# Kernel optimization log

Measured on AMD Instinct MI355X. Metric: run time of the kernel, lower is better.

Reference implementation:

```python
import jax, jax.numpy as jnp
import numpy as np
from jax import lax

LR, SB, LB = 256, 16, 8  # lr_size, spatial_bin, luma_bins
DN = ('NCHW', 'OIHW', 'NCHW')


def conv2d(x, w, b=None, stride=1, pad=1):
    out = lax.conv_general_dilated(x, w, (stride, stride), [(pad, pad), (pad, pad)], dimension_numbers=DN)
    return out if b is None else out + b[None, :, None, None]


def gaussian_blur17(x):
    # kornia GaussianBlur2d(kernel=(17,17), sigma=(2,2)), reflect padding, separable
    t = jnp.arange(17, dtype=x.dtype) - 8.0
    g = jnp.exp(-(t * t) / 8.0)  # 2*sigma^2 = 8
    g = g / g.sum()
    C = x.shape[1]
    xp = jnp.pad(x, ((0, 0), (0, 0), (8, 8), (8, 8)), mode='reflect')
    kh = jnp.broadcast_to(g.reshape(1, 1, 17, 1), (C, 1, 17, 1))
    kw = jnp.broadcast_to(g.reshape(1, 1, 1, 17), (C, 1, 1, 17))
    x1 = lax.conv_general_dilated(xp, kh, (1, 1), 'VALID', dimension_numbers=DN, feature_group_count=C)
    return lax.conv_general_dilated(x1, kw, (1, 1), 'VALID', dimension_numbers=DN, feature_group_count=C)


def nearest_resize(x, size):
    # torch F.interpolate mode='nearest': src = floor(dst * in/out)
    H, W = x.shape[-2], x.shape[-1]
    iy = jnp.floor(jnp.arange(size) * (H / size)).astype(jnp.int32)
    ix = jnp.floor(jnp.arange(size) * (W / size)).astype(jnp.int32)
    return x[:, :, iy][:, :, :, ix]


def grid_sample_3d_border(inp, grid):
    # inp [B,C,D,Hi,Wi]; grid [B,Do,Ho,Wo,3] with (x,y,z); bilinear, padding_mode='border', align_corners=False
    B, C, D, Hi, Wi = inp.shape
    x = jnp.clip(((grid[..., 0] + 1.0) * Wi - 1.0) * 0.5, 0.0, Wi - 1.0)
    y = jnp.clip(((grid[..., 1] + 1.0) * Hi - 1.0) * 0.5, 0.0, Hi - 1.0)
    z = jnp.clip(((grid[..., 2] + 1.0) * D - 1.0) * 0.5, 0.0, D - 1.0)
    x0 = jnp.floor(x); y0 = jnp.floor(y); z0 = jnp.floor(z)
    fx = (x - x0)[:, None]; fy = (y - y0)[:, None]; fz = (z - z0)[:, None]  # [B,1,Do,Ho,Wo]
    x0i = x0.astype(jnp.int32); y0i = y0.astype(jnp.int32); z0i = z0.astype(jnp.int32)
    x1i = jnp.minimum(x0i + 1, Wi - 1); y1i = jnp.minimum(y0i + 1, Hi - 1); z1i = jnp.minimum(z0i + 1, D - 1)
    flat = inp.reshape(B, C, D * Hi * Wi)
    M = grid.shape[1] * grid.shape[2] * grid.shape[3]

    def gat(zi, yi, xi):
        idx = ((zi * Hi + yi) * Wi + xi).reshape(B, 1, M)
        v = jnp.take_along_axis(flat, jnp.broadcast_to(idx, (B, C, M)), axis=2)
        return v.reshape(B, C, grid.shape[1], grid.shape[2], grid.shape[3])

    return (gat(z0i, y0i, x0i) * (1 - fz) * (1 - fy) * (1 - fx)
            + gat(z0i, y0i, x1i) * (1 - fz) * (1 - fy) * fx
            + gat(z0i, y1i, x0i) * (1 - fz) * fy * (1 - fx)
            + gat(z0i, y1i, x1i) * (1 - fz) * fy * fx
            + gat(z1i, y0i, x0i) * fz * (1 - fy) * (1 - fx)
            + gat(z1i, y0i, x1i) * fz * (1 - fy) * fx
            + gat(z1i, y1i, x0i) * fz * fy * (1 - fx)
            + gat(z1i, y1i, x1i) * fz * fy * fx)


def _forward(lqs, evs, gw1, gb1, gw2, gb2, sw0, sb0, sw1, sb1, sw2, sb2, sw3, sb3,
             cw0, cb0, cw1, cb1, fw1, fb1, fw2, fb2, fw3, fb3, lw1, lb1, lw2, fuw, fub):
    B, _, H, W = lqs.shape
    # --- HighresStreamNet guide ---
    g = gaussian_blur17(lqs)
    g = jax.nn.relu(conv2d(g, gw1, gb1, 1, 0))
    guide = jax.nn.sigmoid(conv2d(g, gw2, gb2, 1, 0)) * 2.0 - 0.5  # [B,1,H,W]
    # --- slicing grid (x,y in (-0.5,1.5) per source, z = guide) ---
    gx = (jnp.arange(W, dtype=lqs.dtype) + 0.5) / W * 2.0 - 0.5
    gy = (jnp.arange(H, dtype=lqs.dtype) + 0.5) / H * 2.0 - 0.5
    gyy, gxx = jnp.meshgrid(gy, gx, indexing='ij')
    base = jnp.broadcast_to(jnp.stack([gxx, gyy], -1)[None, None], (B, 1, H, W, 2))
    grid = jnp.concatenate([base, guide[..., None]], axis=-1)  # [B,1,H,W,3]
    # --- LowresStreamNet ---
    lr = nearest_resize(lqs, LR)
    ev = evs if (evs.shape[-1] == LR and evs.shape[-2] == LR) else nearest_resize(evs, LR)
    x = jnp.concatenate([lr, ev], axis=1)  # [B,18,256,256]
    for w_, b_ in ((sw0, sb0), (sw1, sb1), (sw2, sb2), (sw3, sb3)):
        x = jax.nn.relu(conv2d(x, w_, b_, 2, 1))  # -> [B,64,16,16]
    xl = conv2d(jax.nn.relu(conv2d(x, lw1, lb1, 1, 1)), lw2, None, 1, 1)  # local, last conv no bias
    xg = jax.nn.relu(conv2d(x, cw0, cb0, 2, 1))
    xg = jax.nn.relu(conv2d(xg, cw1, cb1, 2, 1)).reshape(B, -1)  # [B,1024]
    xg = jax.nn.relu(xg @ fw1.T + fb1)
    xg = jax.nn.relu(xg @ fw2.T + fb2)
    xg = xg @ fw3.T + fb3  # [B,64]
    fused = jax.nn.relu(xg[:, :, None, None] + xl)
    bg = conv2d(fused, fuw, fub, 1, 0).reshape(B, 1, LB, SB, SB)  # bilateral grid [B,1,8,16,16]
    hr = grid_sample_3d_border(bg, grid)  # [B,1,1,H,W]
    return hr.reshape(B, -1, H, W)


def setup_inputs():
    key = jax.random.key(0)
    ks = iter(jax.random.split(key, 40))

    def W_(shape):
        fan_in = int(np.prod(shape[1:]))
        return jax.random.normal(next(ks), shape, jnp.float32) * np.float32(np.sqrt(2.0 / fan_in))

    def Z(n):
        return jnp.zeros((n,), jnp.float32)

    B, H, Wd = 8, 1024, 1024
    return {
        'lqs': jax.random.uniform(next(ks), (B, 3, H, Wd), jnp.float32),
        'evs': jax.random.normal(next(ks), (B, 15, 256, 256), jnp.float32) * 0.1,
        'gw1': W_((16, 3, 1, 1)), 'gb1': Z(16), 'gw2': W_((1, 16, 1, 1)), 'gb2': Z(1),
        'sw0': W_((8, 18, 3, 3)), 'sb0': Z(8), 'sw1': W_((16, 8, 3, 3)), 'sb1': Z(16),
        'sw2': W_((32, 16, 3, 3)), 'sb2': Z(32), 'sw3': W_((64, 32, 3, 3)), 'sb3': Z(64),
        'cw0': W_((64, 64, 3, 3)), 'cb0': Z(64), 'cw1': W_((64, 64, 3, 3)), 'cb1': Z(64),
        'fw1': W_((256, 1024)), 'fb1': Z(256), 'fw2': W_((128, 256)), 'fb2': Z(128),
        'fw3': W_((64, 128)), 'fb3': Z(64),
        'lw1': W_((64, 64, 3, 3)), 'lb1': Z(64), 'lw2': W_((64, 64, 3, 3)),
        'fuw': W_((8, 64, 1, 1)), 'fub': Z(8),
    }


def reference(lqs, evs, gw1, gb1, gw2, gb2, sw0, sb0, sw1, sb1, sw2, sb2, sw3, sb3,
              cw0, cb0, cw1, cb1, fw1, fb1, fw2, fb2, fw3, fb3, lw1, lb1, lw2, fuw, fub):
    return _forward(lqs, evs, gw1, gb1, gw2, gb2, sw0, sb0, sw1, sb1, sw2, sb2, sw3, sb3,
                    cw0, cb0, cw1, cb1, fw1, fb1, fw2, fb2, fw3, fb3, lw1, lb1, lw2, fuw, fub)
```

## Files before the change

### kernel.cpp

```cpp
#include <hip/hip_runtime.h>
#include <hip/hip_bf16.h>
#include <math.h>

#define BATCH 8
#define HH 1024
#define WW 1024

__device__ __forceinline__ int reflect1024(int i) {
    i = i < 0 ? -i : i;
    return i > 1023 ? 2046 - i : i;
}

__global__ __launch_bounds__(256) void conv0_k(const float* __restrict__ lqs,
                                               const float* __restrict__ evs,
                                               const float* __restrict__ w,
                                               const float* __restrict__ bias,
                                               float* __restrict__ out) {
    int idx = blockIdx.x * 256 + threadIdx.x;
    int q = idx & 4095;
    int b = idx >> 12;
    int qx = q & 31, oy = q >> 5;
    int iy0 = oy * 2 - 1;

    float acc[4][8];
#pragma unroll
    for (int j = 0; j < 4; ++j)
#pragma unroll
        for (int o = 0; o < 8; ++o) acc[j][o] = bias[o];

#pragma unroll
    for (int ic = 0; ic < 3; ++ic) {
        const float* ipc = lqs + (size_t)(b * 3 + ic) * HH * WW;
#pragma unroll
        for (int ky = 0; ky < 3; ++ky) {
            int iy = iy0 + ky;
            if (iy < 0) continue;
            const float* row = ipc + (size_t)iy * 4 * WW;
            float xr[9];
#pragma unroll
            for (int i = 0; i < 9; ++i) {
                int ix = 8 * qx - 1 + i;
                xr[i] = (ix >= 0) ? row[ix * 4] : 0.0f;
            }
#pragma unroll
            for (int o = 0; o < 8; ++o) {
                const float* wp = w + (o * 18 + ic) * 9 + ky * 3;
#pragma unroll
                for (int j = 0; j < 4; ++j)
#pragma unroll
                    for (int kx = 0; kx < 3; ++kx)
                        acc[j][o] = fmaf(wp[kx], xr[2 * j + kx], acc[j][o]);
            }
        }
    }
    for (int ic = 0; ic < 15; ++ic) {
        const float* ipc = evs + (size_t)(b * 15 + ic) * 65536;
#pragma unroll
        for (int ky = 0; ky < 3; ++ky) {
            int iy = iy0 + ky;
            if (iy < 0) continue;
            const float* row = ipc + iy * 256;
            const float4* r4 = (const float4*)row;
            float4 A = r4[2 * qx];
            float4 Bv = r4[2 * qx + 1];
            float m = (qx > 0) ? row[8 * qx - 1] : 0.0f;
            float xr[9] = {m, A.x, A.y, A.z, A.w, Bv.x, Bv.y, Bv.z, Bv.w};
#pragma unroll
            for (int o = 0; o < 8; ++o) {
                const float* wp = w + (o * 18 + ic + 3) * 9 + ky * 3;
#pragma unroll
                for (int j = 0; j < 4; ++j)
#pragma unroll
                    for (int kx = 0; kx < 3; ++kx)
                        acc[j][o] = fmaf(wp[kx], xr[2 * j + kx], acc[j][o]);
            }
        }
    }
#pragma unroll
    for (int o = 0; o < 8; ++o) {
        float4 v = make_float4(fmaxf(acc[0][o], 0.0f), fmaxf(acc[1][o], 0.0f),
                               fmaxf(acc[2][o], 0.0f), fmaxf(acc[3][o], 0.0f));
        *(float4*)(out + ((size_t)(b * 8 + o) << 14) + oy * 128 + qx * 4) = v;
    }
}

template <int IC, int OC, int OCT, int IH, int IW, int STRIDE, bool RELU, bool HASB>
__global__ __launch_bounds__(256) void convN_k(const float* __restrict__ in,
                                               const float* __restrict__ w,
                                               const float* __restrict__ bias,
                                               float* __restrict__ out) {
    constexpr int OH = (IH + 2 - 3) / STRIDE + 1;
    constexpr int OW = (IW + 2 - 3) / STRIDE + 1;
    constexpr int POS = OH * OW;
    constexpr int G = OC / OCT;
    int idx = blockIdx.x * 256 + threadIdx.x;
    if (idx >= BATCH * G * POS) return;
    int px = idx % POS;
    int g = (idx / POS) % G;
    int b = idx / (POS * G);
    int ox = px % OW, oy = px / OW;
    int iy0 = oy * STRIDE - 1, ix0 = ox * STRIDE - 1;

    float acc[OCT];
#pragma unroll
    for (int o = 0; o < OCT; ++o) acc[o] = HASB ? bias[g * OCT + o] : 0.0f;

    const float* ip = in + (size_t)b * IC * IH * IW;
    for (int ic = 0; ic < IC; ++ic) {
        const float* ipc = ip + ic * IH * IW;
        float x[9];
#pragma unroll
        for (int ky = 0; ky < 3; ++ky) {
            int iy = iy0 + ky;
#pragma unroll
            for (int kx = 0; kx < 3; ++kx) {
                int ix = ix0 + kx;
                bool ok = (iy >= 0) && (iy < IH) && (ix >= 0) && (ix < IW);
                x[ky * 3 + kx] = ok ? ipc[iy * IW + ix] : 0.0f;
            }
        }
#pragma unroll
        for (int o = 0; o < OCT; ++o) {
            const float* wp = w + ((g * OCT + o) * IC + ic) * 9;
#pragma unroll
            for (int k = 0; k < 9; ++k) acc[o] = fmaf(wp[k], x[k], acc[o]);
        }
    }
#pragma unroll
    for (int o = 0; o < OCT; ++o) {
        float v = acc[o];
        if (RELU) v = fmaxf(v, 0.0f);
        out[(size_t)(b * OC + g * OCT + o) * POS + px] = v;
    }
}

template <int IC, int OC, int OCT, int IH, int IW, int STRIDE, int SPLIT>
__global__ __launch_bounds__(256) void convS_k(const float* __restrict__ in,
                                               const float* __restrict__ w,
                                               float* __restrict__ part) {
    constexpr int OH = (IH + 2 - 3) / STRIDE + 1;
    constexpr int OW = (IW + 2 - 3) / STRIDE + 1;
    constexpr int POS = OH * OW;
    constexpr int G = OC / OCT;
    constexpr int TOT = BATCH * G * POS;
    constexpr int ICS = IC / SPLIT;
    constexpr int N = BATCH * OC * POS;
    int idx = blockIdx.x * 256 + threadIdx.x;
    if (idx >= TOT * SPLIT) return;
    int s = idx / TOT, r = idx % TOT;
    int px = r % POS;
    int g = (r / POS) % G;
    int b = r / (POS * G);
    int ox = px % OW, oy = px / OW;
    int iy0 = oy * STRIDE - 1, ix0 = ox * STRIDE - 1;

    float acc[OCT];
#pragma unroll
    for (int o = 0; o < OCT; ++o) acc[o] = 0.0f;

    const float* ip = in + (size_t)b * IC * IH * IW;
    for (int ic = s * ICS; ic < (s + 1) * ICS; ++ic) {
        const float* ipc = ip + ic * IH * IW;
        float x[9];
#pragma unroll
        for (int ky = 0; ky < 3; ++ky) {
            int iy = iy0 + ky;
#pragma unroll
            for (int kx = 0; kx < 3; ++kx) {
                int ix = ix0 + kx;
                bool ok = (iy >= 0) && (iy < IH) && (ix >= 0) && (ix < IW);
                x[ky * 3 + kx] = ok ? ipc[iy * IW + ix] : 0.0f;
            }
        }
#pragma unroll
        for (int o = 0; o < OCT; ++o) {
            const float* wp = w + ((g * OCT + o) * IC + ic) * 9;
#pragma unroll
            for (int k = 0; k < 9; ++k) acc[o] = fmaf(wp[k], x[k], acc[o]);
        }
    }
#pragma unroll
    for (int o = 0; o < OCT; ++o)
        part[(size_t)s * N + (size_t)(b * OC + g * OCT + o) * POS + px] = acc[o];
}

template <int OC, int POS, int SPLIT, bool RELU, bool HASB>
__global__ __launch_bounds__(256) void reduce_k(const float* __restrict__ part,
                                                const float* __restrict__ bias,
                                                float* __restrict__ out) {
    constexpr int N = BATCH * OC * POS;
    int idx = blockIdx.x * 256 + threadIdx.x;
    if (idx >= N) return;
    int oc = (idx / POS) % OC;
    float a = HASB ? bias[oc] : 0.0f;
#pragma unroll
    for (int s = 0; s < SPLIT; ++s) a += part[(size_t)s * N + idx];
    out[idx] = RELU ? fmaxf(a, 0.0f) : a;
}

__global__ __launch_bounds__(256) void fc1_k(const float* __restrict__ part_cw1,
                                             const float* __restrict__ cb1,
                                             const float* __restrict__ fw1,
                                             const float* __restrict__ fb1,
                                             float* __restrict__ h1) {
    __shared__ float xin[1024];
    int t = threadIdx.x;
    int b = blockIdx.x >> 6;
    int rgrp = blockIdx.x & 63;
    int wave = t >> 6, lane = t & 63;

    for (int i = t; i < 1024; i += 256) {
        float v = cb1[i >> 4];
#pragma unroll
        for (int s = 0; s < 16; ++s) v += part_cw1[s * 8192 + b * 1024 + i];
        xin[i] = fmaxf(v, 0.0f);
    }
    __syncthreads();

    int r = (rgrp << 2) | wave;
    const float4* w4 = (const float4*)(fw1 + r * 1024);
    const float4* x4 = (const float4*)xin;
    float acc = 0.0f;
#pragma unroll
    for (int jj = 0; jj < 4; ++jj) {
        float4 wv = w4[lane + 64 * jj];
        float4 xv = x4[lane + 64 * jj];
        acc = fmaf(wv.x, xv.x, acc);
        acc = fmaf(wv.y, xv.y, acc);
        acc = fmaf(wv.z, xv.z, acc);
        acc = fmaf(wv.w, xv.w, acc);
    }
#pragma unroll
    for (int m = 32; m; m >>= 1) acc += __shfl_xor(acc, m, 64);
    if (lane == 0) h1[b * 256 + r] = fmaxf(acc + fb1[r], 0.0f);
}

__global__ __launch_bounds__(256) void fc2_k(const float* __restrict__ h1,
                                             const float* __restrict__ fw2,
                                             const float* __restrict__ fb2,
                                             float* __restrict__ h2) {
    int t = threadIdx.x;
    int b = blockIdx.x >> 5;
    int rgrp = blockIdx.x & 31;
    int wave = t >> 6, lane = t & 63;
    int r = (rgrp << 2) | wave;
    float4 wv = ((const float4*)(fw2 + r * 256))[lane];
    float4 xv = ((const float4*)(h1 + b * 256))[lane];
    float acc = fmaf(wv.x, xv.x, fmaf(wv.y, xv.y, fmaf(wv.z, xv.z, wv.w * xv.w)));
#pragma unroll
    for (int m = 32; m; m >>= 1) acc += __shfl_xor(acc, m, 64);
    if (lane == 0) h2[b * 128 + r] = fmaxf(acc + fb2[r], 0.0f);
}

__global__ __launch_bounds__(256) void fc3_k(const float* __restrict__ h2,
                                             const float* __restrict__ fw3,
                                             const float* __restrict__ fb3,
                                             float* __restrict__ xgv) {
    int t = threadIdx.x;
    int b = blockIdx.x >> 4;
    int rgrp = blockIdx.x & 15;
    int wave = t >> 6, lane = t & 63;
    int r = (rgrp << 2) | wave;
    float2 wv = ((const float2*)(fw3 + r * 128))[lane];
    float2 xv = ((const float2*)(h2 + b * 128))[lane];
    float acc = fmaf(wv.x, xv.x, wv.y * xv.y);
#pragma unroll
    for (int m = 32; m; m >>= 1) acc += __shfl_xor(acc, m, 64);
    if (lane == 0) xgv[b * 64 + r] = acc + fb3[r];
}

__global__ __launch_bounds__(256) void fuse_k(const float* __restrict__ xg,
                                              const float* __restrict__ part_lw2,
                                              const float* __restrict__ fuw,
                                              const float* __restrict__ fub,
                                              float* __restrict__ bg) {
    int px = threadIdx.x;
    int d = blockIdx.x & 7;
    int b = blockIdx.x >> 3;
    float acc = fub[d];
    for (int c = 0; c < 64; ++c) {
        int base = (b * 64 + c) * 256 + px;
        float xlv = 0.0f;
#pragma unroll
        for (int s = 0; s < 8; ++s) xlv += part_lw2[s * 131072 + base];
        float f = fmaxf(xg[b * 64 + c] + xlv, 0.0f);
        acc = fmaf(fuw[d * 64 + c], f, acc);
    }
    bg[(b * 8 + d) * 256 + px] = acc;
}

__global__ __launch_bounds__(256) void guide_slice_k(const float* __restrict__ lqs,
                                                     const float* __restrict__ bgp,
                                                     const float* __restrict__ gw1,
                                                     const float* __restrict__ gb1,
                                                     const float* __restrict__ gw2,
                                                     const float* __restrict__ gb2,
                                                     float* __restrict__ out) {
    constexpr int TW = 64, TH = 32;
    __shared__ float sBH[3][TH][81];
    __shared__ float sBG[2048];
    __shared__ float sW1[48], sB1[16], sW2[16], sB2v[1];

    int t = threadIdx.x;
    int bx = blockIdx.x & 15;
    int by = (blockIdx.x >> 4) & 31;
    int b = blockIdx.x >> 9;
    int x0 = bx * TW, y0 = by * TH;

    float gv[17];
    {
        float gs = 0.0f;
#pragma unroll
        for (int i = 0; i < 17; ++i) {
            float d = (float)i - 8.0f;
            gv[i] = expf(-(d * d) * 0.125f);
            gs += gv[i];
        }
        float inv = 1.0f / gs;
#pragma unroll
        for (int i = 0; i < 17; ++i) gv[i] *= inv;
    }

    for (int i = t; i < 2048; i += 256) sBG[i] = bgp[b * 2048 + i];
    if (t < 48) sW1[t] = gw1[t];
    if (t < 16) { sB1[t] = gb1[t]; sW2[t] = gw2[t]; }
    if (t == 0) sB2v[0] = gb2[0];

    if (t < 240) {
        int c = t / 80, xo = t % 80;
        int gx = reflect1024(x0 + xo - 8);
        const float* colp = lqs + (size_t)(b * 3 + c) * HH * WW + gx;
        float win[17];
#pragma unroll
        for (int i = 0; i < 16; ++i)
            win[i] = colp[(size_t)reflect1024(y0 - 8 + i) * WW];
#pragma unroll
        for (int j = 0; j < TH; ++j) {
            win[(16 + j) % 17] = colp[(size_t)reflect1024(y0 + 8 + j) * WW];
            float acc = 0.0f;
#pragma unroll
            for (int i = 0; i < 17; ++i) acc = fmaf(gv[i], win[(j + i) % 17], acc);
            sBH[c][j][xo] = acc;
        }
    }
    __syncthreads();

    int yy = t >> 3, xs = (t & 7) * 8;
    int Y = y0 + yy;
    float fy = fminf(fmaxf((Y + 0.5f) * (1.0f / 64.0f) + 3.5f, 0.0f), 15.0f);
    float yf = floorf(fy);
    int yi = (int)yf;
    float ay = fy - yf;
    int yi1 = min(yi + 1, 15);

    float bcv[3][8];
#pragma unroll
    for (int c = 0; c < 3; ++c) {
        float win[17];
#pragma unroll
        for (int i = 0; i < 16; ++i) win[i] = sBH[c][yy][xs + i];
#pragma unroll
        for (int j = 0; j < 8; ++j) {
            win[(16 + j) % 17] = sBH[c][yy][xs + 16 + j];
            float acc = 0.0f;
#pragma unroll
            for (int i = 0; i < 17; ++i) acc = fmaf(gv[i], win[(j + i) % 17], acc);
            bcv[c][j] = acc;
        }
    }

    float val[8];
#pragma unroll
    for (int j = 0; j < 8; ++j) {
        float b0 = bcv[0][j], b1 = bcv[1][j], b2 = bcv[2][j];
        float s = sB2v[0];
#pragma unroll
        for (int c = 0; c < 16; ++c) {
            float g1 = fmaf(sW1[c * 3 + 0], b0,
                       fmaf(sW1[c * 3 + 1], b1,
                       fmaf(sW1[c * 3 + 2], b2, sB1[c])));
            s = fmaf(sW2[c], fmaxf(g1, 0.0f), s);
        }
        float sig = 1.0f / (1.0f + expf(-s));
        float guide = sig * 2.0f - 0.5f;

        int X = x0 + xs + j;
        float fx = fminf(fmaxf((X + 0.5f) * (1.0f / 64.0f) + 3.5f, 0.0f), 15.0f);
        float fz = fminf(fmaxf(fmaf(guide, 4.0f, 3.5f), 0.0f), 7.0f);
        float xf = floorf(fx), zf = floorf(fz);
        int xi = (int)xf, zi = (int)zf;
        float ax = fx - xf, az = fz - zf;
        int xi1 = min(xi + 1, 15), zi1 = min(zi + 1, 7);

        const float* g0 = sBG + zi * 256;
        const float* g1p = sBG + zi1 * 256;
        int i00 = yi * 16 + xi, i01 = yi * 16 + xi1;
        int i10 = yi1 * 16 + xi, i11 = yi1 * 16 + xi1;
        float c00 = g0[i00] + az * (g1p[i00] - g0[i00]);
        float c01 = g0[i01] + az * (g1p[i01] - g0[i01]);
        float c10 = g0[i10] + az * (g1p[i10] - g0[i10]);
        float c11 = g0[i11] + az * (g1p[i11] - g0[i11]);
        float c0 = c00 + ay * (c10 - c00);
        float c1 = c01 + ay * (c11 - c01);
        val[j] = c0 + ax * (c1 - c0);
    }
    float4* op = (float4*)(out + (size_t)b * HH * WW + (size_t)Y * WW + x0 + xs);
    op[0] = make_float4(val[0], val[1], val[2], val[3]);
    op[1] = make_float4(val[4], val[5], val[6], val[7]);
}

extern "C" void kernel_launch(void* const* d_in, const int* in_sizes, int n_in,
                              void* d_out, int out_size, void* d_ws, size_t ws_size,
                              hipStream_t stream) {
    const float* lqs = (const float*)d_in[0];
    const float* evs = (const float*)d_in[1];
    const float* gw1 = (const float*)d_in[2];
    const float* gb1 = (const float*)d_in[3];
    const float* gw2 = (const float*)d_in[4];
    const float* gb2 = (const float*)d_in[5];
    const float* sw0 = (const float*)d_in[6];
    const float* sb0 = (const float*)d_in[7];
    const float* sw1 = (const float*)d_in[8];
    const float* sb1 = (const float*)d_in[9];
    const float* sw2 = (const float*)d_in[10];
    const float* sb2 = (const float*)d_in[11];
    const float* sw3 = (const float*)d_in[12];
    const float* sb3 = (const float*)d_in[13];
    const float* cw0 = (const float*)d_in[14];
    const float* cb0 = (const float*)d_in[15];
    const float* cw1 = (const float*)d_in[16];
    const float* cb1 = (const float*)d_in[17];
    const float* fw1 = (const float*)d_in[18];
    const float* fb1 = (const float*)d_in[19];
    const float* fw2 = (const float*)d_in[20];
    const float* fb2 = (const float*)d_in[21];
    const float* fw3 = (const float*)d_in[22];
    const float* fb3 = (const float*)d_in[23];
    const float* lw1 = (const float*)d_in[24];
    const float* lb1 = (const float*)d_in[25];
    const float* lw2 = (const float*)d_in[26];
    const float* fuw = (const float*)d_in[27];
    const float* fub = (const float*)d_in[28];
    float* out = (float*)d_out;

    float* ws = (float*)d_ws;
    float* o0 = ws;
    float* o1 = o0 + 1048576;
    float* o2 = o1 + 524288;
    float* o3 = o2 + 262144;
    float* xl1 = o3 + 131072;
    float* xg0 = xl1 + 131072;
    float* xgv = xg0 + 32768;
    float* bg = xgv + 512;
    float* h1 = bg + 16384;
    float* h2 = h1 + 2048;
    float* partA = h2 + 1024;
    float* part_lw2 = partA + 1048576;
    float* part_cw1 = part_lw2 + 1048576;

    conv0_k<<<128, 256, 0, stream>>>(lqs, evs, sw0, sb0, o0);
    convN_k<8, 16, 8, 128, 128, 2, true, true><<<256, 256, 0, stream>>>(o0, sw1, sb1, o1);
    convS_k<16, 32, 8, 64, 64, 2, 4><<<512, 256, 0, stream>>>(o1, sw2, partA);
    reduce_k<32, 1024, 4, true, true><<<1024, 256, 0, stream>>>(partA, sb2, o2);
    convS_k<32, 64, 8, 32, 32, 2, 8><<<512, 256, 0, stream>>>(o2, sw3, partA);
    reduce_k<64, 256, 8, true, true><<<512, 256, 0, stream>>>(partA, sb3, o3);
    convS_k<64, 64, 8, 16, 16, 1, 8><<<512, 256, 0, stream>>>(o3, lw1, partA);
    reduce_k<64, 256, 8, true, true><<<512, 256, 0, stream>>>(partA, lb1, xl1);
    convS_k<64, 64, 8, 16, 16, 1, 8><<<512, 256, 0, stream>>>(xl1, lw2, part_lw2);
    convS_k<64, 64, 8, 16, 16, 2, 16><<<256, 256, 0, stream>>>(o3, cw0, partA);
    reduce_k<64, 64, 16, true, true><<<128, 256, 0, stream>>>(partA, cb0, xg0);
    convS_k<64, 64, 4, 8, 8, 2, 16><<<128, 256, 0, stream>>>(xg0, cw1, part_cw1);
    fc1_k<<<512, 256, 0, stream>>>(part_cw1, cb1, fw1, fb1, h1);
    fc2_k<<<256, 256, 0, stream>>>(h1, fw2, fb2, h2);
    fc3_k<<<128, 256, 0, stream>>>(h2, fw3, fb3, xgv);
    fuse_k<<<64, 256, 0, stream>>>(xgv, part_lw2, fuw, fub, bg);
    guide_slice_k<<<BATCH * 32 * 16, 256, 0, stream>>>(lqs, bg, gw1, gb1, gw2, gb2, out);
}
```

Before: 397.2 us.

## Fuse low-res conv/FC pipeline into one cooperative persistent kernel with grid syncs

Replaces the chain of sixteen small conv, split-reduce, FC and fuse kernels with a single cooperative kernel of 512 blocks that runs each stage and separates them with grid-wide syncs. The split-K partial buffers and reduce kernels are removed; each thread now computes full-IC outputs with fewer output channels per thread. The FC layers and fuse step run inside eight blocks using shared memory. This targets launch overhead and the extra partial-sum traffic, but gives up parallelism in later stages and adds grid-sync cost.

```diff
diff --git a/kernel.cpp b/kernel.cpp
--- a/kernel.cpp
+++ b/kernel.cpp
@@ -1,153 +1,93 @@
 #include <hip/hip_runtime.h>
+#include <hip/hip_cooperative_groups.h>
 #include <hip/hip_bf16.h>
 #include <math.h>
+
+namespace cg = cooperative_groups;
 
 #define BATCH 8
 #define HH 1024
 #define WW 1024
 
+#define NBLK 512
+#define NTHR 131072
+
 __device__ __forceinline__ int reflect1024(int i) {
     i = i < 0 ? -i : i;
     return i > 1023 ? 2046 - i : i;
 }
 
-__global__ __launch_bounds__(256) void conv0_k(const float* __restrict__ lqs,
-                                               const float* __restrict__ evs,
-                                               const float* __restrict__ w,
-                                               const float* __restrict__ bias,
-                                               float* __restrict__ out) {
-    int idx = blockIdx.x * 256 + threadIdx.x;
-    int q = idx & 4095;
-    int b = idx >> 12;
-    int qx = q & 31, oy = q >> 5;
-    int iy0 = oy * 2 - 1;
-
-    float acc[4][8];
-#pragma unroll
-    for (int j = 0; j < 4; ++j)
-#pragma unroll
-        for (int o = 0; o < 8; ++o) acc[j][o] = bias[o];
+struct MegaArgs {
+    const float *lqs, *evs;
+    const float *sw0, *sb0, *sw1, *sb1, *sw2, *sb2, *sw3, *sb3;
+    const float *lw1, *lb1, *lw2;
+    const float *cw0, *cb0, *cw1, *cb1;
+    const float *fw1, *fb1, *fw2, *fb2, *fw3, *fb3;
+    const float *fuw, *fub;
+    float *o0, *o1, *o2, *o3, *xl1, *xl2, *xg0, *xin, *bg;
+};
+
+__device__ __forceinline__ void stage_conv0(int idx, const MegaArgs& A) {
+    int px = idx & 16383;
+    int b = idx >> 14;
+    int ox = px & 127, oy = px >> 7;
+    int iy0 = 2 * oy - 1, ix0 = 2 * ox - 1;
+
+    float acc[8];
+#pragma unroll
+    for (int o = 0; o < 8; ++o) acc[o] = A.sb0[o];
 
 #pragma unroll
     for (int ic = 0; ic < 3; ++ic) {
-        const float* ipc = lqs + (size_t)(b * 3 + ic) * HH * WW;
+        const float* ipc = A.lqs + ((size_t)(b * 3 + ic) << 20);
 #pragma unroll
         for (int ky = 0; ky < 3; ++ky) {
             int iy = iy0 + ky;
-            if (iy < 0) continue;
+            if ((unsigned)iy >= 256u) continue;
             const float* row = ipc + (size_t)iy * 4 * WW;
-            float xr[9];
-#pragma unroll
-            for (int i = 0; i < 9; ++i) {
-                int ix = 8 * qx - 1 + i;
-                xr[i] = (ix >= 0) ? row[ix * 4] : 0.0f;
-            }
-#pragma unroll
-            for (int o = 0; o < 8; ++o) {
-                const float* wp = w + (o * 18 + ic) * 9 + ky * 3;
-#pragma unroll
-                for (int j = 0; j < 4; ++j)
-#pragma unroll
-                    for (int kx = 0; kx < 3; ++kx)
-                        acc[j][o] = fmaf(wp[kx], xr[2 * j + kx], acc[j][o]);
+#pragma unroll
+            for (int kx = 0; kx < 3; ++kx) {
+                int ix = ix0 + kx;
+                if ((unsigned)ix >= 256u) continue;
+                float v = row[ix * 4];
+                const float* wp = A.sw0 + ic * 9 + ky * 3 + kx;
+#pragma unroll
+                for (int o = 0; o < 8; ++o) acc[o] = fmaf(wp[o * 162], v, acc[o]);
             }
         }
     }
     for (int ic = 0; ic < 15; ++ic) {
-        const float* ipc = evs + (size_t)(b * 15 + ic) * 65536;
+        const float* ipc = A.evs + ((size_t)(b * 15 + ic) << 16);
 #pragma unroll
         for (int ky = 0; ky < 3; ++ky) {
             int iy = iy0 + ky;
-            if (iy < 0) continue;
+            if ((unsigned)iy >= 256u) continue;
             const float* row = ipc + iy * 256;
-            const float4* r4 = (const float4*)row;
-            float4 A = r4[2 * qx];
-            float4 Bv = r4[2 * qx + 1];
-            float m = (qx > 0) ? row[8 * qx - 1] : 0.0f;
-            float xr[9] = {m, A.x, A.y, A.z, A.w, Bv.x, Bv.y, Bv.z, Bv.w};
-#pragma unroll
-            for (int o = 0; o < 8; ++o) {
-                const float* wp = w + (o * 18 + ic + 3) * 9 + ky * 3;
-#pragma unroll
-                for (int j = 0; j < 4; ++j)
-#pragma unroll
-                    for (int kx = 0; kx < 3; ++kx)
-                        acc[j][o] = fmaf(wp[kx], xr[2 * j + kx], acc[j][o]);
-            }
-        }
-    }
-#pragma unroll
-    for (int o = 0; o < 8; ++o) {
-        float4 v = make_float4(fmaxf(acc[0][o], 0.0f), fmaxf(acc[1][o], 0.0f),
-                               fmaxf(acc[2][o], 0.0f), fmaxf(acc[3][o], 0.0f));
-        *(float4*)(out + ((size_t)(b * 8 + o) << 14) + oy * 128 + qx * 4) = v;
-    }
+#pragma unroll
+            for (int kx = 0; kx < 3; ++kx) {
+                int ix = ix0 + kx;
+                if ((unsigned)ix >= 256u) continue;
+                float v = row[ix];
+                const float* wp = A.sw0 + (ic + 3) * 9 + ky * 3 + kx;
+#pragma unroll
+                for (int o = 0; o < 8; ++o) acc[o] = fmaf(wp[o * 162], v, acc[o]);
+            }
+        }
+    }
+#pragma unroll
+    for (int o = 0; o < 8; ++o)
+        A.o0[((size_t)(b * 8 + o) << 14) + px] = fmaxf(acc[o], 0.0f);
 }
 
 template <int IC, int OC, int OCT, int IH, int IW, int STRIDE, bool RELU, bool HASB>
-__global__ __launch_bounds__(256) void convN_k(const float* __restrict__ in,
-                                               const float* __restrict__ w,
-                                               const float* __restrict__ bias,
-                                               float* __restrict__ out) {
+__device__ __forceinline__ void stage_conv(int r, const float* __restrict__ in,
+                                           const float* __restrict__ w,
+                                           const float* __restrict__ bias,
+                                           float* __restrict__ out) {
     constexpr int OH = (IH + 2 - 3) / STRIDE + 1;
     constexpr int OW = (IW + 2 - 3) / STRIDE + 1;
     constexpr int POS = OH * OW;
     constexpr int G = OC / OCT;
-    int idx = blockIdx.x * 256 + threadIdx.x;
-    if (idx >= BATCH * G * POS) return;
-    int px = idx % POS;
-    int g = (idx / POS) % G;
-    int b = idx / (POS * G);
-    int ox = px % OW, oy = px / OW;
-    int iy0 = oy * STRIDE - 1, ix0 = ox * STRIDE - 1;
-
-    float acc[OCT];
-#pragma unroll
-    for (int o = 0; o < OCT; ++o) acc[o] = HASB ? bias[g * OCT + o] : 0.0f;
-
-    const float* ip = in + (size_t)b * IC * IH * IW;
-    for (int ic = 0; ic < IC; ++ic) {
-        const float* ipc = ip + ic * IH * IW;
-        float x[9];
-#pragma unroll
-        for (int ky = 0; ky < 3; ++ky) {
-            int iy = iy0 + ky;
-#pragma unroll
-            for (int kx = 0; kx < 3; ++kx) {
-                int ix = ix0 + kx;
-                bool ok = (iy >= 0) && (iy < IH) && (ix >= 0) && (ix < IW);
-                x[ky * 3 + kx] = ok ? ipc[iy * IW + ix] : 0.0f;
-            }
-        }
-#pragma unroll
-        for (int o = 0; o < OCT; ++o) {
-            const float* wp = w + ((g * OCT + o) * IC + ic) * 9;
-#pragma unroll
-            for (int k = 0; k < 9; ++k) acc[o] = fmaf(wp[k], x[k], acc[o]);
-        }
-    }
-#pragma unroll
-    for (int o = 0; o < OCT; ++o) {
-        float v = acc[o];
-        if (RELU) v = fmaxf(v, 0.0f);
-        out[(size_t)(b * OC + g * OCT + o) * POS + px] = v;
-    }
-}
-
-template <int IC, int OC, int OCT, int IH, int IW, int STRIDE, int SPLIT>
-__global__ __launch_bounds__(256) void convS_k(const float* __restrict__ in,
-                                               const float* __restrict__ w,
-                                               float* __restrict__ part) {
-    constexpr int OH = (IH + 2 - 3) / STRIDE + 1;
-    constexpr int OW = (IW + 2 - 3) / STRIDE + 1;
-    constexpr int POS = OH * OW;
-    constexpr int G = OC / OCT;
-    constexpr int TOT = BATCH * G * POS;
-    constexpr int ICS = IC / SPLIT;
-    constexpr int N = BATCH * OC * POS;
-    int idx = blockIdx.x * 256 + threadIdx.x;
-    if (idx >= TOT * SPLIT) return;
-    int s = idx / TOT, r = idx % TOT;
     int px = r % POS;
     int g = (r / POS) % G;
     int b = r / (POS * G);
@@ -156,10 +96,10 @@
 
     float acc[OCT];
 #pragma unroll
-    for (int o = 0; o < OCT; ++o) acc[o] = 0.0f;
+    for (int o = 0; o < OCT; ++o) acc[o] = HASB ? bias[g * OCT + o] : 0.0f;
 
     const float* ip = in + (size_t)b * IC * IH * IW;
-    for (int ic = s * ICS; ic < (s + 1) * ICS; ++ic) {
+    for (int ic = 0; ic < IC; ++ic) {
         const float* ipc = ip + ic * IH * IW;
         float x[9];
 #pragma unroll
@@ -168,7 +108,7 @@
 #pragma unroll
             for (int kx = 0; kx < 3; ++kx) {
                 int ix = ix0 + kx;
-                bool ok = (iy >= 0) && (iy < IH) && (ix >= 0) && (ix < IW);
+                bool ok = ((unsigned)iy < (unsigned)IH) && ((unsigned)ix < (unsigned)IW);
                 x[ky * 3 + kx] = ok ? ipc[iy * IW + ix] : 0.0f;
             }
         }
@@ -180,113 +120,101 @@
         }
     }
 #pragma unroll
-    for (int o = 0; o < OCT; ++o)
-        part[(size_t)s * N + (size_t)(b * OC + g * OCT + o) * POS + px] = acc[o];
-}
-
-template <int OC, int POS, int SPLIT, bool RELU, bool HASB>
-__global__ __launch_bounds__(256) void reduce_k(const float* __restrict__ part,
-                                                const float* __restrict__ bias,
-                                                float* __restrict__ out) {
-    constexpr int N = BATCH * OC * POS;
+    for (int o = 0; o < OCT; ++o) {
+        float v = acc[o];
+        if (RELU) v = fmaxf(v, 0.0f);
+        out[(size_t)(b * OC + g * OCT + o) * POS + px] = v;
+    }
+}
+
+__global__ __launch_bounds__(256, 2) void mega_k(MegaArgs A) {
+    cg::grid_group grid = cg::this_grid();
     int idx = blockIdx.x * 256 + threadIdx.x;
-    if (idx >= N) return;
-    int oc = (idx / POS) % OC;
-    float a = HASB ? bias[oc] : 0.0f;
-#pragma unroll
-    for (int s = 0; s < SPLIT; ++s) a += part[(size_t)s * N + idx];
-    out[idx] = RELU ? fmaxf(a, 0.0f) : a;
-}
-
-__global__ __launch_bounds__(256) void fc1_k(const float* __restrict__ part_cw1,
-                                             const float* __restrict__ cb1,
-                                             const float* __restrict__ fw1,
-                                             const float* __restrict__ fb1,
-                                             float* __restrict__ h1) {
-    __shared__ float xin[1024];
-    int t = threadIdx.x;
-    int b = blockIdx.x >> 6;
-    int rgrp = blockIdx.x & 63;
-    int wave = t >> 6, lane = t & 63;
-
-    for (int i = t; i < 1024; i += 256) {
-        float v = cb1[i >> 4];
-#pragma unroll
-        for (int s = 0; s < 16; ++s) v += part_cw1[s * 8192 + b * 1024 + i];
-        xin[i] = fmaxf(v, 0.0f);
-    }
-    __syncthreads();
-
-    int r = (rgrp << 2) | wave;
-    const float4* w4 = (const float4*)(fw1 + r * 1024);
-    const float4* x4 = (const float4*)xin;
-    float acc = 0.0f;
-#pragma unroll
-    for (int jj = 0; jj < 4; ++jj) {
-        float4 wv = w4[lane + 64 * jj];
-        float4 xv = x4[lane + 64 * jj];
-        acc = fmaf(wv.x, xv.x, acc);
-        acc = fmaf(wv.y, xv.y, acc);
-        acc = fmaf(wv.z, xv.z, acc);
-        acc = fmaf(wv.w, xv.w, acc);
-    }
-#pragma unroll
-    for (int m = 32; m; m >>= 1) acc += __shfl_xor(acc, m, 64);
-    if (lane == 0) h1[b * 256 + r] = fmaxf(acc + fb1[r], 0.0f);
-}
-
-__global__ __launch_bounds__(256) void fc2_k(const float* __restrict__ h1,
-                                             const float* __restrict__ fw2,
-                                             const float* __restrict__ fb2,
-                                             float* __restrict__ h2) {
-    int t = threadIdx.x;
-    int b = blockIdx.x >> 5;
-    int rgrp = blockIdx.x & 31;
-    int wave = t >> 6, lane = t & 63;
-    int r = (rgrp << 2) | wave;
-    float4 wv = ((const float4*)(fw2 + r * 256))[lane];
-    float4 xv = ((const float4*)(h1 + b * 256))[lane];
-    float acc = fmaf(wv.x, xv.x, fmaf(wv.y, xv.y, fmaf(wv.z, xv.z, wv.w * xv.w)));
-#pragma unroll
-    for (int m = 32; m; m >>= 1) acc += __shfl_xor(acc, m, 64);
-    if (lane == 0) h2[b * 128 + r] = fmaxf(acc + fb2[r], 0.0f);
-}
-
-__global__ __launch_bounds__(256) void fc3_k(const float* __restrict__ h2,
-                                             const float* __restrict__ fw3,
-                                             const float* __restrict__ fb3,
-                                             float* __restrict__ xgv) {
-    int t = threadIdx.x;
-    int b = blockIdx.x >> 4;
-    int rgrp = blockIdx.x & 15;
-    int wave = t >> 6, lane = t & 63;
-    int r = (rgrp << 2) | wave;
-    float2 wv = ((const float2*)(fw3 + r * 128))[lane];
-    float2 xv = ((const float2*)(h2 + b * 128))[lane];
-    float acc = fmaf(wv.x, xv.x, wv.y * xv.y);
-#pragma unroll
-    for (int m = 32; m; m >>= 1) acc += __shfl_xor(acc, m, 64);
-    if (lane == 0) xgv[b * 64 + r] = acc + fb3[r];
-}
-
-__global__ __launch_bounds__(256) void fuse_k(const float* __restrict__ xg,
-                                              const float* __restrict__ part_lw2,
-                                              const float* __restrict__ fuw,
-                                              const float* __restrict__ fub,
-                                              float* __restrict__ bg) {
-    int px = threadIdx.x;
-    int d = blockIdx.x & 7;
-    int b = blockIdx.x >> 3;
-    float acc = fub[d];
-    for (int c = 0; c < 64; ++c) {
-        int base = (b * 64 + c) * 256 + px;
-        float xlv = 0.0f;
-#pragma unroll
-        for (int s = 0; s < 8; ++s) xlv += part_lw2[s * 131072 + base];
-        float f = fmaxf(xg[b * 64 + c] + xlv, 0.0f);
-        acc = fmaf(fuw[d * 64 + c], f, acc);
-    }
-    bg[(b * 8 + d) * 256 + px] = acc;
+
+    stage_conv0(idx, A);
+    grid.sync();
+
+    stage_conv<8, 16, 4, 128, 128, 2, true, true>(idx, A.o0, A.sw1, A.sb1, A.o1);
+    grid.sync();
+
+    stage_conv<16, 32, 2, 64, 64, 2, true, true>(idx, A.o1, A.sw2, A.sb2, A.o2);
+    grid.sync();
+
+    stage_conv<32, 64, 1, 32, 32, 2, true, true>(idx, A.o2, A.sw3, A.sb3, A.o3);
+    grid.sync();
+
+    stage_conv<64, 64, 1, 16, 16, 1, true, true>(idx, A.o3, A.lw1, A.lb1, A.xl1);
+    if (idx < 32768)
+        stage_conv<64, 64, 1, 16, 16, 2, true, true>(idx, A.o3, A.cw0, A.cb0, A.xg0);
+    grid.sync();
+
+    stage_conv<64, 64, 1, 16, 16, 1, false, false>(idx, A.xl1, A.lw2, nullptr, A.xl2);
+    if (idx < 8192)
+        stage_conv<64, 64, 1, 8, 8, 2, true, true>(idx, A.xg0, A.cw1, A.cb1, A.xin);
+    grid.sync();
+
+    __shared__ __align__(16) float sX[1024];
+    __shared__ __align__(16) float sH1[256];
+    __shared__ __align__(16) float sH2[128];
+    __shared__ float sXG[64];
+    if (blockIdx.x < 8) {
+        int b = blockIdx.x, t = threadIdx.x;
+#pragma unroll
+        for (int j = 0; j < 4; ++j) sX[t + 256 * j] = A.xin[b * 1024 + t + 256 * j];
+        __syncthreads();
+        {
+            const float4* w4 = (const float4*)(A.fw1 + (size_t)t * 1024);
+            const float4* x4 = (const float4*)sX;
+            float a[4] = {0.f, 0.f, 0.f, 0.f};
+#pragma unroll 4
+            for (int j = 0; j < 256; ++j) {
+                float4 wv = w4[j], xv = x4[j];
+                a[j & 3] = fmaf(wv.x, xv.x, fmaf(wv.y, xv.y,
+                           fmaf(wv.z, xv.z, fmaf(wv.w, xv.w, a[j & 3]))));
+            }
+            sH1[t] = fmaxf(a[0] + a[1] + a[2] + a[3] + A.fb1[t], 0.0f);
+        }
+        __syncthreads();
+        if (t < 128) {
+            const float4* w4 = (const float4*)(A.fw2 + (size_t)t * 256);
+            const float4* x4 = (const float4*)sH1;
+            float a[4] = {0.f, 0.f, 0.f, 0.f};
+#pragma unroll 4
+            for (int j = 0; j < 64; ++j) {
+                float4 wv = w4[j], xv = x4[j];
+                a[j & 3] = fmaf(wv.x, xv.x, fmaf(wv.y, xv.y,
+                           fmaf(wv.z, xv.z, fmaf(wv.w, xv.w, a[j & 3]))));
+            }
+            sH2[t] = fmaxf(a[0] + a[1] + a[2] + a[3] + A.fb2[t], 0.0f);
+        }
+        __syncthreads();
+        if (t < 64) {
+            const float4* w4 = (const float4*)(A.fw3 + (size_t)t * 128);
+            const float4* x4 = (const float4*)sH2;
+            float a[4] = {0.f, 0.f, 0.f, 0.f};
+#pragma unroll 4
+            for (int j = 0; j < 32; ++j) {
+                float4 wv = w4[j], xv = x4[j];
+                a[j & 3] = fmaf(wv.x, xv.x, fmaf(wv.y, xv.y,
+                           fmaf(wv.z, xv.z, fmaf(wv.w, xv.w, a[j & 3]))));
+            }
+            sXG[t] = a[0] + a[1] + a[2] + a[3] + A.fb3[t];
+        }
+        __syncthreads();
+        {
+            int px = t;
+            float accd[8];
+#pragma unroll
+            for (int d = 0; d < 8; ++d) accd[d] = A.fub[d];
+            for (int c = 0; c < 64; ++c) {
+                float f = fmaxf(sXG[c] + A.xl2[(size_t)(b * 64 + c) * 256 + px], 0.0f);
+#pragma unroll
+                for (int d = 0; d < 8; ++d) accd[d] = fmaf(A.fuw[d * 64 + c], f, accd[d]);
+            }
+#pragma unroll
+            for (int d = 0; d < 8; ++d) A.bg[(b * 8 + d) * 256 + px] = accd[d];
+        }
+    }
 }
 
 __global__ __launch_bounds__(256) void guide_slice_k(const float* __restrict__ lqs,
@@ -444,35 +372,28 @@
     float* out = (float*)d_out;
 
     float* ws = (float*)d_ws;
-    float* o0 = ws;
-    float* o1 = o0 + 1048576;
-    float* o2 = o1 + 524288;
-    float* o3 = o2 + 262144;
+    float* o0  = ws;
+    float* o1  = o0 + 1048576;
+    float* o2  = o1 + 524288;
+    float* o3  = o2 + 262144;
     float* xl1 = o3 + 131072;
-    float* xg0 = xl1 + 131072;
-    float* xgv = xg0 + 32768;
-    float* bg = xgv + 512;
-    float* h1 = bg + 16384;
-    float* h2 = h1 + 2048;
-    float* partA = h2 + 1024;
-    float* part_lw2 = partA + 1048576;
-    float* part_cw1 = part_lw2 + 1048576;
-
-    conv0_k<<<128, 256, 0, stream>>>(lqs, evs, sw0, sb0, o0);
-    convN_k<8, 16, 8, 128, 128, 2, true, true><<<256, 256, 0, stream>>>(o0, sw1, sb1, o1);
-    convS_k<16, 32, 8, 64, 64, 2, 4><<<512, 256, 0, stream>>>(o1, sw2, partA);
-    reduce_k<32, 1024, 4, true, true><<<1024, 256, 0, stream>>>(partA, sb2, o2);
-    convS_k<32, 64, 8, 32, 32, 2, 8><<<512, 256, 0, stream>>>(o2, sw3, partA);
-    reduce_k<64, 256, 8, true, true><<<512, 256, 0, stream>>>(partA, sb3, o3);
-    convS_k<64, 64, 8, 16, 16, 1, 8><<<512, 256, 0, stream>>>(o3, lw1, partA);
-    reduce_k<64, 256, 8, true, true><<<512, 256, 0, stream>>>(partA, lb1, xl1);
-    convS_k<64, 64, 8, 16, 16, 1, 8><<<512, 256, 0, stream>>>(xl1, lw2, part_lw2);
-    convS_k<64, 64, 8, 16, 16, 2, 16><<<256, 256, 0, stream>>>(o3, cw0, partA);
-    reduce_k<64, 64, 16, true, true><<<128, 256, 0, stream>>>(partA, cb0, xg0);
-    convS_k<64, 64, 4, 8, 8, 2, 16><<<128, 256, 0, stream>>>(xg0, cw1, part_cw1);
-    fc1_k<<<512, 256, 0, stream>>>(part_cw1, cb1, fw1, fb1, h1);
-    fc2_k<<<256, 256, 0, stream>>>(h1, fw2, fb2, h2);
-    fc3_k<<<128, 256, 0, stream>>>(h2, fw3, fb3, xgv);
-    fuse_k<<<64, 256, 0, stream>>>(xgv, part_lw2, fuw, fub, bg);
+    float* xl2 = xl1 + 131072;
+    float* xg0 = xl2 + 131072;
+    float* xin = xg0 + 32768;
+    float* bg  = xin + 8192;
+
+    MegaArgs A;
+    A.lqs = lqs; A.evs = evs;
+    A.sw0 = sw0; A.sb0 = sb0; A.sw1 = sw1; A.sb1 = sb1;
+    A.sw2 = sw2; A.sb2 = sb2; A.sw3 = sw3; A.sb3 = sb3;
+    A.lw1 = lw1; A.lb1 = lb1; A.lw2 = lw2;
+    A.cw0 = cw0; A.cb0 = cb0; A.cw1 = cw1; A.cb1 = cb1;
+    A.fw1 = fw1; A.fb1 = fb1; A.fw2 = fw2; A.fb2 = fb2;
+    A.fw3 = fw3; A.fb3 = fb3; A.fuw = fuw; A.fub = fub;
+    A.o0 = o0; A.o1 = o1; A.o2 = o2; A.o3 = o3;
+    A.xl1 = xl1; A.xl2 = xl2; A.xg0 = xg0; A.xin = xin; A.bg = bg;
+
+    void* params[] = {(void*)&A};
+    hipLaunchCooperativeKernel(mega_k, dim3(NBLK), dim3(256), params, 0, stream);
     guide_slice_k<<<BATCH * 32 * 16, 256, 0, stream>>>(lqs, bg, gw1, gb1, gw2, gb2, out);
 }
```

New measurement: 888.1 us. 124% more time.
